# Performance work log

Measured on AMD Instinct MI355X. Metric: run time of the kernel, lower is better.

Reference implementation:

```python
import jax, jax.numpy as jnp
import numpy as np

THRESHOLD = 1.0
CURRENT_DECAY = 0.3
VOLTAGE_DECAY = 0.25
TAU_GRAD = 0.001  # surrogate-gradient sharpness (SLAYER escape-rate style)


@jax.custom_vjp
def spike(v):
    return (v >= THRESHOLD).astype(v.dtype)


def _spike_fwd(v):
    return spike(v), v


def _spike_bwd(v, g):
    # SLAYER-style surrogate: dS/dv = exp(-|v - theta| / tau) / tau
    return (g * jnp.exp(-jnp.abs(v - THRESHOLD) / TAU_GRAD) / TAU_GRAD,)


spike.defvjp(_spike_fwd, _spike_bwd)


def weight_norm(v, g):
    # torch weight_norm(dim=0): w = g * v / ||v|| with norm over all non-output dims
    axes = tuple(range(1, v.ndim))
    n = jnp.sqrt(jnp.sum(v * v, axis=axes, keepdims=True))
    return g.reshape((-1,) + (1,) * (v.ndim - 1)) * v / n


def cuba(z):
    # CUBA LIF dynamics over trailing time axis.  z: (B, ..., T)
    zt = jnp.moveaxis(z, -1, 0)  # (T, B, ...)

    def step(carry, z_t):
        c, v = carry
        c = (1.0 - CURRENT_DECAY) * c + z_t
        v = (1.0 - VOLTAGE_DECAY) * v + c
        s = spike(v)
        v = v * (1.0 - s)  # hard reset to zero on spike
        return (c, v), s

    init = (jnp.zeros_like(zt[0]), jnp.zeros_like(zt[0]))
    _, s = jax.lax.scan(step, init, zt)
    return jnp.moveaxis(s, 0, -1)  # (B, ..., T)


def conv2d_t(x, w):
    # Apply 2D conv independently per timestep. x: (B,C,H,W,T), w: (O,I,5,5)
    B, C, H, W, T = x.shape
    xb = jnp.moveaxis(x, -1, 1).reshape(B * T, C, H, W)
    y = jax.lax.conv_general_dilated(
        xb, w, window_strides=(4, 4), padding=[(1, 1), (1, 1)],
        dimension_numbers=('NCHW', 'OIHW', 'NCHW'))
    O, Ho, Wo = y.shape[1], y.shape[2], y.shape[3]
    return jnp.moveaxis(y.reshape(B, T, O, Ho, Wo), 1, -1)  # (B,O,Ho,Wo,T)


def dense_t(x, w):
    # x: (B, I, T), w: (O, I)
    return jnp.einsum('bit,oi->bot', x, w)


def setup_inputs() -> dict:
    key = jax.random.key(0)
    ks = jax.random.split(key, 8)
    B, T = 16, 64
    # sparse binary event input (DVS-like spikes)
    x = (jax.random.uniform(ks[0], (B, 2, 128, 128, T)) < 0.2).astype(jnp.float32)

    def mk(k, shape):
        fan_in = int(np.prod(shape[1:]))
        return jax.random.normal(k, shape, jnp.float32) / np.sqrt(fan_in)

    # weight_norm direction v; gain g absorbs weight_scale=2 (||w_eff|| = 2 per filter)
    return {
        'x': x,
        'conv1_v': mk(ks[1], (8, 2, 5, 5)),   'conv1_g': jnp.full((8,), 2.0, jnp.float32),
        'conv2_v': mk(ks[2], (32, 8, 5, 5)),  'conv2_g': jnp.full((32,), 2.0, jnp.float32),
        'conv3_v': mk(ks[3], (64, 32, 5, 5)), 'conv3_g': jnp.full((64,), 2.0, jnp.float32),
        'dense1_v': mk(ks[4], (2056, 256)),   'dense1_g': jnp.full((2056,), 2.0, jnp.float32),
        'dense2_v': mk(ks[5], (11, 2056)),    'dense2_g': jnp.full((11,), 2.0, jnp.float32),
    }


def reference(x, conv1_v, conv1_g, conv2_v, conv2_g, conv3_v, conv3_g,
              dense1_v, dense1_g, dense2_v, dense2_g):
    B = x.shape[0]
    T = x.shape[-1]
    # conv blocks: synapse then CUBA neuron
    for v, g in ((conv1_v, conv1_g), (conv2_v, conv2_g), (conv3_v, conv3_g)):
        x = cuba(conv2d_t(x, weight_norm(v, g)))
    # flatten (C,H,W) -> features; (B,64,2,2,T) -> (B,256,T)
    x = x.reshape(B, 64 * 2 * 2, T)
    for v, g in ((dense1_v, dense1_g), (dense2_v, dense2_g)):
        x = cuba(dense_t(x, weight_norm(v, g)))
    return x  # (B, 11, T) output spike train
```

## Files before the change

kernel.cpp:

```cpp
#include <hip/hip_runtime.h>
#include <cstddef>

#define TT 64

#define RFL(x) __builtin_amdgcn_readfirstlane(x)

typedef unsigned long long u64;

__device__ __forceinline__ void scanc(float& c, float& v, float& z) {
    c = fmaf(0.7f, c, z);
    v = fmaf(0.75f, v, c);
    float s = (v >= 1.0f) ? 1.0f : 0.0f;
    v = (v >= 1.0f) ? 0.0f : v;
    z = s;
}
__device__ __forceinline__ void scan4(float& c, float& v, float4& a) {
    scanc(c, v, a.x); scanc(c, v, a.y); scanc(c, v, a.z); scanc(c, v, a.w);
}
__device__ __forceinline__ float bit2f(u64 m, int t) {
    return (float)((m >> t) & 1ULL);
}

__global__ __launch_bounds__(256) void prep(
    const float* __restrict__ c1v, const float* __restrict__ c1g, float* __restrict__ w1T,
    const float* __restrict__ c2v, const float* __restrict__ c2g, float* __restrict__ w2T,
    const float* __restrict__ c3v, const float* __restrict__ c3g, float* __restrict__ w3T,
    const float* __restrict__ d1v, const float* __restrict__ d1g, float* __restrict__ wd1,
    const float* __restrict__ d2v, const float* __restrict__ d2g, float* __restrict__ wd2P,
    const float* __restrict__ x, u64* __restrict__ xb) {
    __shared__ float red[256];
    const int bid = blockIdx.x;
    if (bid >= 2171) {
        const int sub = threadIdx.x & 15;
        const int grp = threadIdx.x >> 4;
        const int pb = bid - 2171;
#pragma unroll
        for (int it = 0; it < 4; it++) {
            const size_t base = ((size_t)pb * 4 + it) * 32;
            const size_t p0 = base + grp;
            const size_t p1 = base + 16 + grp;
            const float4 v0 = *(const float4*)(x + p0 * TT + sub * 4);
            const float4 v1 = *(const float4*)(x + p1 * TT + sub * 4);
            const unsigned int n0 = (v0.x > 0.5f ? 1u : 0u) | (v0.y > 0.5f ? 2u : 0u) |
                                    (v0.z > 0.5f ? 4u : 0u) | (v0.w > 0.5f ? 8u : 0u);
            const unsigned int n1 = (v1.x > 0.5f ? 1u : 0u) | (v1.y > 0.5f ? 2u : 0u) |
                                    (v1.z > 0.5f ? 4u : 0u) | (v1.w > 0.5f ? 8u : 0u);
            u64 w0 = (u64)n0 << (4 * sub);
            u64 w1 = (u64)n1 << (4 * sub);
            w0 |= __shfl_xor(w0, 1); w1 |= __shfl_xor(w1, 1);
            w0 |= __shfl_xor(w0, 2); w1 |= __shfl_xor(w1, 2);
            w0 |= __shfl_xor(w0, 4); w1 |= __shfl_xor(w1, 4);
            w0 |= __shfl_xor(w0, 8); w1 |= __shfl_xor(w1, 8);
            if (sub == 0) { xb[p0] = w0; xb[p1] = w1; }
        }
        return;
    }
    const float *v, *g; float* w; int o, K, LD; bool tr;
    if (bid < 8)         { v = c1v; g = c1g; w = w1T;  o = bid;        K = 50;   LD = 8;  tr = true;  }
    else if (bid < 40)   { v = c2v; g = c2g; w = w2T;  o = bid - 8;    K = 200;  LD = 32; tr = true;  }
    else if (bid < 104)  { v = c3v; g = c3g; w = w3T;  o = bid - 40;   K = 800;  LD = 64; tr = true;  }
    else if (bid < 2160) { v = d1v; g = d1g; w = wd1;  o = bid - 104;  K = 256;  LD = 0;  tr = false; }
    else                 { v = d2v; g = d2g; w = wd2P; o = bid - 2160; K = 2056; LD = 12; tr = true;  }

    float s = 0.f;
    for (int k = threadIdx.x; k < K; k += 256) {
        float xx = v[(size_t)o * K + k];
        s += xx * xx;
    }
    red[threadIdx.x] = s;
    __syncthreads();
    for (int off = 128; off > 0; off >>= 1) {
        if (threadIdx.x < off) red[threadIdx.x] += red[threadIdx.x + off];
        __syncthreads();
    }
    const float scale = g[o] / sqrtf(red[0]);
    for (int k = threadIdx.x; k < K; k += 256) {
        float val = scale * v[(size_t)o * K + k];
        if (tr) w[(size_t)k * LD + o] = val;
        else    w[(size_t)o * K + k] = val;
    }
}

__global__ __launch_bounds__(256) void conv1_cuba(const u64* __restrict__ xb,
                                                  const float* __restrict__ w1T,
                                                  u64* __restrict__ s1b) {
    __shared__ float lds[4][8][68];
    const int wid = RFL(threadIdx.x >> 6), t = threadIdx.x & 63;
    const int task = RFL(blockIdx.x) * 4 + wid;
    const int spi = task & 1023, b = task >> 10;
    const int oy = spi >> 5, ox = spi & 31;

    float a0=0,a1=0,a2=0,a3=0,a4=0,a5=0,a6=0,a7=0;
    const u64* xq = xb + (size_t)b * 2 * 16384;

    if (oy >= 1 && ox >= 1) {
        const u64* xi = xq + (size_t)(oy * 4 - 1) * 128 + (ox * 4 - 1);
        for (int ci = 0; ci < 2; ci++) {
            u64 m[25];
#pragma unroll
            for (int ky = 0; ky < 5; ky++)
#pragma unroll
                for (int kx = 0; kx < 5; kx++)
                    m[ky * 5 + kx] = xi[ci * 16384 + ky * 128 + kx];
#pragma unroll
            for (int k = 0; k < 25; k++) {
                const float xvk = bit2f(m[k], t);
                const float4* wp = (const float4*)(w1T + (ci * 25 + k) * 8);
                const float4 wA = wp[0], wB = wp[1];
                a0 = fmaf(wA.x, xvk, a0); a1 = fmaf(wA.y, xvk, a1);
                a2 = fmaf(wA.z, xvk, a2); a3 = fmaf(wA.w, xvk, a3);
                a4 = fmaf(wB.x, xvk, a4); a5 = fmaf(wB.y, xvk, a5);
                a6 = fmaf(wB.z, xvk, a6); a7 = fmaf(wB.w, xvk, a7);
            }
        }
    } else {
        for (int ci = 0; ci < 2; ci++) {
#pragma unroll
            for (int ky = 0; ky < 5; ky++) {
                const int iy = oy * 4 + ky - 1;
                if (iy < 0 || iy >= 128) continue;
#pragma unroll
                for (int kx = 0; kx < 5; kx++) {
                    const int ix = ox * 4 + kx - 1;
                    if (ix < 0 || ix >= 128) continue;
                    const float xvk = bit2f(xq[ci * 16384 + iy * 128 + ix], t);
                    const float4* wp = (const float4*)(w1T + (ci * 25 + ky * 5 + kx) * 8);
                    const float4 wA = wp[0], wB = wp[1];
                    a0 = fmaf(wA.x, xvk, a0); a1 = fmaf(wA.y, xvk, a1);
                    a2 = fmaf(wA.z, xvk, a2); a3 = fmaf(wA.w, xvk, a3);
                    a4 = fmaf(wB.x, xvk, a4); a5 = fmaf(wB.y, xvk, a5);
                    a6 = fmaf(wB.z, xvk, a6); a7 = fmaf(wB.w, xvk, a7);
                }
            }
        }
    }
    lds[wid][0][t] = a0; lds[wid][1][t] = a1; lds[wid][2][t] = a2; lds[wid][3][t] = a3;
    lds[wid][4][t] = a4; lds[wid][5][t] = a5; lds[wid][6][t] = a6; lds[wid][7][t] = a7;
    __syncthreads();
    if (t < 8) {
        float* row = &lds[wid][t][0];
        float c = 0.f, v = 0.f;
        for (int tc = 0; tc < 4; tc++) {
            float4 r0 = *(const float4*)&row[tc * 16 + 0];
            float4 r1 = *(const float4*)&row[tc * 16 + 4];
            float4 r2 = *(const float4*)&row[tc * 16 + 8];
            float4 r3 = *(const float4*)&row[tc * 16 + 12];
            scan4(c, v, r0); scan4(c, v, r1); scan4(c, v, r2); scan4(c, v, r3);
            *(float4*)&row[tc * 16 + 0] = r0; *(float4*)&row[tc * 16 + 4] = r1;
            *(float4*)&row[tc * 16 + 8] = r2; *(float4*)&row[tc * 16 + 12] = r3;
        }
    }
    __syncthreads();
    u64* ob = s1b + (size_t)b * 8 * 1024 + spi;
#pragma unroll
    for (int ch = 0; ch < 8; ch++) {
        const u64 m = __ballot(lds[wid][ch][t] > 0.5f);
        if (t == 0) ob[(size_t)ch * 1024] = m;
    }
}

__global__ __launch_bounds__(256) void conv2_cuba(const u64* __restrict__ s1b,
                                                  const float* __restrict__ w2T,
                                                  float* __restrict__ s2) {
    __shared__ float lds[4][16][68];
    const int wid = RFL(threadIdx.x >> 6), t = threadIdx.x & 63;
    const int task = RFL(blockIdx.x) * 4 + wid;
    const int og = task & 1;
    const int spi = (task >> 1) & 63;
    const int b = task >> 7;
    const int oy = spi >> 3, ox = spi & 7;

    float a[16];
#pragma unroll
    for (int j = 0; j < 16; j++) a[j] = 0.f;
    const u64* sb = s1b + (size_t)b * 8 * 1024;

    if (oy >= 1 && ox >= 1) {
        const u64* si = sb + (size_t)(oy * 4 - 1) * 32 + (ox * 4 - 1);
        for (int ci = 0; ci < 8; ci++) {
            u64 m[25];
#pragma unroll
            for (int ky = 0; ky < 5; ky++)
#pragma unroll
                for (int kx = 0; kx < 5; kx++)
                    m[ky * 5 + kx] = si[ci * 1024 + ky * 32 + kx];
#pragma unroll
            for (int k = 0; k < 25; k++) {
                const float xvk = bit2f(m[k], t);
                const float4* wp = (const float4*)(w2T + (ci * 25 + k) * 32 + og * 16);
                const float4 w0 = wp[0], w1 = wp[1], w2 = wp[2], w3 = wp[3];
                a[0]  = fmaf(w0.x, xvk, a[0]);  a[1]  = fmaf(w0.y, xvk, a[1]);
                a[2]  = fmaf(w0.z, xvk, a[2]);  a[3]  = fmaf(w0.w, xvk, a[3]);
                a[4]  = fmaf(w1.x, xvk, a[4]);  a[5]  = fmaf(w1.y, xvk, a[5]);
                a[6]  = fmaf(w1.z, xvk, a[6]);  a[7]  = fmaf(w1.w, xvk, a[7]);
                a[8]  = fmaf(w2.x, xvk, a[8]);  a[9]  = fmaf(w2.y, xvk, a[9]);
                a[10] = fmaf(w2.z, xvk, a[10]); a[11] = fmaf(w2.w, xvk, a[11]);
                a[12] = fmaf(w3.x, xvk, a[12]); a[13] = fmaf(w3.y, xvk, a[13]);
                a[14] = fmaf(w3.z, xvk, a[14]); a[15] = fmaf(w3.w, xvk, a[15]);
            }
        }
    } else {
        for (int ci = 0; ci < 8; ci++) {
#pragma unroll
            for (int ky = 0; ky < 5; ky++) {
                const int iy = oy * 4 + ky - 1;
                if (iy < 0 || iy >= 32) continue;
#pragma unroll
                for (int kx = 0; kx < 5; kx++) {
                    const int ix = ox * 4 + kx - 1;
                    if (ix < 0 || ix >= 32) continue;
                    const float xvk = bit2f(sb[ci * 1024 + iy * 32 + ix], t);
                    const float4* wp =
                        (const float4*)(w2T + (ci * 25 + ky * 5 + kx) * 32 + og * 16);
                    const float4 w0 = wp[0], w1 = wp[1], w2 = wp[2], w3 = wp[3];
                    a[0]  = fmaf(w0.x, xvk, a[0]);  a[1]  = fmaf(w0.y, xvk, a[1]);
                    a[2]  = fmaf(w0.z, xvk, a[2]);  a[3]  = fmaf(w0.w, xvk, a[3]);
                    a[4]  = fmaf(w1.x, xvk, a[4]);  a[5]  = fmaf(w1.y, xvk, a[5]);
                    a[6]  = fmaf(w1.z, xvk, a[6]);  a[7]  = fmaf(w1.w, xvk, a[7]);
                    a[8]  = fmaf(w2.x, xvk, a[8]);  a[9]  = fmaf(w2.y, xvk, a[9]);
                    a[10] = fmaf(w2.z, xvk, a[10]); a[11] = fmaf(w2.w, xvk, a[11]);
                    a[12] = fmaf(w3.x, xvk, a[12]); a[13] = fmaf(w3.y, xvk, a[13]);
                    a[14] = fmaf(w3.z, xvk, a[14]); a[15] = fmaf(w3.w, xvk, a[15]);
                }
            }
        }
    }
#pragma unroll
    for (int j = 0; j < 16; j++) lds[wid][j][t] = a[j];
    __syncthreads();
    if (t < 16) {
        const float* row = &lds[wid][t][0];
        float4* op = (float4*)(s2 + (((size_t)b * 32 + og * 16 + t) * 64 + spi) * TT);
        float c = 0.f, v = 0.f;
        for (int tc = 0; tc < 4; tc++) {
            float4 r0 = *(const float4*)&row[tc * 16 + 0];
            float4 r1 = *(const float4*)&row[tc * 16 + 4];
            float4 r2 = *(const float4*)&row[tc * 16 + 8];
            float4 r3 = *(const float4*)&row[tc * 16 + 12];
            scan4(c, v, r0); scan4(c, v, r1); scan4(c, v, r2); scan4(c, v, r3);
            op[tc * 4 + 0] = r0; op[tc * 4 + 1] = r1;
            op[tc * 4 + 2] = r2; op[tc * 4 + 3] = r3;
        }
    }
}

template <int OY, int OX>
__device__ __forceinline__ void conv3_acc(const float* __restrict__ xb,
                                          const float* __restrict__ wTo,
                                          int wid, float* __restrict__ acc) {
    constexpr int KY0 = (OY == 0) ? 1 : 0;
    constexpr int KX0 = (OX == 0) ? 1 : 0;
    constexpr int NKY = 5 - KY0;
    constexpr int NKX = 5 - KX0;
    for (int c8 = 0; c8 < 8; c8++) {
        const int ci = wid * 8 + c8;
        float xv[NKY * NKX];
#pragma unroll
        for (int ky = KY0; ky < 5; ky++) {
#pragma unroll
            for (int kx = KX0; kx < 5; kx++) {
                const int iy = OY * 4 + ky - 1;
                const int ix = OX * 4 + kx - 1;
                xv[(ky - KY0) * NKX + (kx - KX0)] =
                    xb[((size_t)((ci * 8 + iy) * 8 + ix)) * TT];
            }
        }
#pragma unroll
        for (int ky = KY0; ky < 5; ky++) {
#pragma unroll
            for (int kx = KX0; kx < 5; kx++) {
                const float xvk = xv[(ky - KY0) * NKX + (kx - KX0)];
                const float4* wp = (const float4*)(wTo + (ci * 25 + ky * 5 + kx) * 64);
                const float4 wA = wp[0], wB = wp[1];
                acc[0] = fmaf(wA.x, xvk, acc[0]); acc[1] = fmaf(wA.y, xvk, acc[1]);
                acc[2] = fmaf(wA.z, xvk, acc[2]); acc[3] = fmaf(wA.w, xvk, acc[3]);
                acc[4] = fmaf(wB.x, xvk, acc[4]); acc[5] = fmaf(wB.y, xvk, acc[5]);
                acc[6] = fmaf(wB.z, xvk, acc[6]); acc[7] = fmaf(wB.w, xvk, acc[7]);
            }
        }
    }
}

__global__ __launch_bounds__(256) void conv3_cuba(const float* __restrict__ s2,
                                                  const float* __restrict__ wT,
                                                  float* __restrict__ s3) {
    __shared__ float red[4][8][68];
    const int wid = RFL(threadIdx.x >> 6), t = threadIdx.x & 63;
    const int og = RFL(blockIdx.x) & 7;
    const int spi = (RFL(blockIdx.x) >> 3) & 3;
    const int b = RFL(blockIdx.x) >> 5;

    float acc[8];
#pragma unroll
    for (int j = 0; j < 8; j++) acc[j] = 0.f;
    const float* xb = s2 + (size_t)b * 32 * 8 * 8 * TT + t;
    const float* wTo = wT + og * 8;

    switch (spi) {
        case 0: conv3_acc<0, 0>(xb, wTo, wid, acc); break;
        case 1: conv3_acc<0, 1>(xb, wTo, wid, acc); break;
        case 2: conv3_acc<1, 0>(xb, wTo, wid, acc); break;
        default: conv3_acc<1, 1>(xb, wTo, wid, acc); break;
    }
#pragma unroll
    for (int j = 0; j < 8; j++) red[wid][j][t] = acc[j];
    __syncthreads();
    if (wid == 0) {
#pragma unroll
        for (int j = 0; j < 8; j++)
            red[0][j][t] = ((red[0][j][t] + red[1][j][t]) + red[2][j][t]) + red[3][j][t];
    }
    __syncthreads();
    if (threadIdx.x < 8) {
        const int j = threadIdx.x;
        const float* row = &red[0][j][0];
        float4* op = (float4*)(s3 + ((size_t)b * 256 + og * 32 + j * 4 + spi) * TT);
        float c = 0.f, v = 0.f;
        for (int tc = 0; tc < 4; tc++) {
            float4 r0 = *(const float4*)&row[tc * 16 + 0];
            float4 r1 = *(const float4*)&row[tc * 16 + 4];
            float4 r2 = *(const float4*)&row[tc * 16 + 8];
            float4 r3 = *(const float4*)&row[tc * 16 + 12];
            scan4(c, v, r0); scan4(c, v, r1); scan4(c, v, r2); scan4(c, v, r3);
            op[tc * 4 + 0] = r0; op[tc * 4 + 1] = r1;
            op[tc * 4 + 2] = r2; op[tc * 4 + 3] = r3;
        }
    }
}

__global__ __launch_bounds__(256) void dense1_cuba(const float* __restrict__ s3,
                                                   const float* __restrict__ w,
                                                   float* __restrict__ s4) {
    __shared__ float lds[4][8][68];
    const int wid = threadIdx.x >> 6, t = threadIdx.x & 63;
    const int task = blockIdx.x * 4 + wid;
    const int bq = task / 257;
    const int ogq = task - bq * 257;
    const int b = RFL(bq);
    const int o0 = RFL(ogq * 8);

    float a0=0,a1=0,a2=0,a3=0,a4=0,a5=0,a6=0,a7=0;
    const float* ab = s3 + (size_t)b * 256 * TT + t;
    const float* r0 = w + (size_t)(o0 + 0) * 256;
    const float* r1 = w + (size_t)(o0 + 1) * 256;
    const float* r2 = w + (size_t)(o0 + 2) * 256;
    const float* r3 = w + (size_t)(o0 + 3) * 256;
    const float* r4 = w + (size_t)(o0 + 4) * 256;
    const float* r5 = w + (size_t)(o0 + 5) * 256;
    const float* r6 = w + (size_t)(o0 + 6) * 256;
    const float* r7 = w + (size_t)(o0 + 7) * 256;

#pragma unroll 2
    for (int i = 0; i < 256; i += 4) {
        const float av0 = ab[(size_t)(i + 0) * TT];
        const float av1 = ab[(size_t)(i + 1) * TT];
        const float av2 = ab[(size_t)(i + 2) * TT];
        const float av3 = ab[(size_t)(i + 3) * TT];
        const float4 q0 = *(const float4*)(r0 + i);
        const float4 q1 = *(const float4*)(r1 + i);
        const float4 q2 = *(const float4*)(r2 + i);
        const float4 q3 = *(const float4*)(r3 + i);
        const float4 q4 = *(const float4*)(r4 + i);
        const float4 q5 = *(const float4*)(r5 + i);
        const float4 q6 = *(const float4*)(r6 + i);
        const float4 q7 = *(const float4*)(r7 + i);
        a0 = fmaf(q0.x, av0, a0); a1 = fmaf(q1.x, av0, a1);
        a2 = fmaf(q2.x, av0, a2); a3 = fmaf(q3.x, av0, a3);
        a4 = fmaf(q4.x, av0, a4); a5 = fmaf(q5.x, av0, a5);
        a6 = fmaf(q6.x, av0, a6); a7 = fmaf(q7.x, av0, a7);
        a0 = fmaf(q0.y, av1, a0); a1 = fmaf(q1.y, av1, a1);
        a2 = fmaf(q2.y, av1, a2); a3 = fmaf(q3.y, av1, a3);
        a4 = fmaf(q4.y, av1, a4); a5 = fmaf(q5.y, av1, a5);
        a6 = fmaf(q6.y, av1, a6); a7 = fmaf(q7.y, av1, a7);
        a0 = fmaf(q0.z, av2, a0); a1 = fmaf(q1.z, av2, a1);
        a2 = fmaf(q2.z, av2, a2); a3 = fmaf(q3.z, av2, a3);
        a4 = fmaf(q4.z, av2, a4); a5 = fmaf(q5.z, av2, a5);
        a6 = fmaf(q6.z, av2, a6); a7 = fmaf(q7.z, av2, a7);
        a0 = fmaf(q0.w, av3, a0); a1 = fmaf(q1.w, av3, a1);
        a2 = fmaf(q2.w, av3, a2); a3 = fmaf(q3.w, av3, a3);
        a4 = fmaf(q4.w, av3, a4); a5 = fmaf(q5.w, av3, a5);
        a6 = fmaf(q6.w, av3, a6); a7 = fmaf(q7.w, av3, a7);
    }
    lds[wid][0][t] = a0; lds[wid][1][t] = a1; lds[wid][2][t] = a2; lds[wid][3][t] = a3;
    lds[wid][4][t] = a4; lds[wid][5][t] = a5; lds[wid][6][t] = a6; lds[wid][7][t] = a7;
    __syncthreads();
    if (t < 8) {
        const float* row = &lds[wid][t][0];
        float4* op = (float4*)(s4 + ((size_t)b * 2056 + o0 + t) * TT);
        float c = 0.f, v = 0.f;
        for (int tc = 0; tc < 4; tc++) {
            float4 r0q = *(const float4*)&row[tc * 16 + 0];
            float4 r1q = *(const float4*)&row[tc * 16 + 4];
            float4 r2q = *(const float4*)&row[tc * 16 + 8];
            float4 r3q = *(const float4*)&row[tc * 16 + 12];
            scan4(c, v, r0q); scan4(c, v, r1q); scan4(c, v, r2q); scan4(c, v, r3q);
            op[tc * 4 + 0] = r0q; op[tc * 4 + 1] = r1q;
            op[tc * 4 + 2] = r2q; op[tc * 4 + 3] = r3q;
        }
    }
}

__global__ __launch_bounds__(256) void dense2_part(const float* __restrict__ s4,
                                                   const float* __restrict__ wP,
                                                   float* __restrict__ z4p) {
    __shared__ float red[4][11][64];
    const int sp = blockIdx.x, b = blockIdx.y;
    const int w = threadIdx.x >> 6, t = threadIdx.x & 63;
    const int i0 = sp * 129;
    const int iend = (i0 + 129 < 2056) ? i0 + 129 : 2056;
    const float* src = s4 + (size_t)b * 2056 * TT + t;

    float acc[11];
#pragma unroll
    for (int j = 0; j < 11; j++) acc[j] = 0.f;

#pragma unroll 4
    for (int i = i0 + w; i < iend; i += 4) {
        const float xv = src[(size_t)i * TT];
        const float4* wp = (const float4*)(wP + (size_t)i * 12);
        const float4 w0 = wp[0], w1 = wp[1], w2 = wp[2];
        acc[0]  = fmaf(w0.x, xv, acc[0]);  acc[1]  = fmaf(w0.y, xv, acc[1]);
        acc[2]  = fmaf(w0.z, xv, acc[2]);  acc[3]  = fmaf(w0.w, xv, acc[3]);
        acc[4]  = fmaf(w1.x, xv, acc[4]);  acc[5]  = fmaf(w1.y, xv, acc[5]);
        acc[6]  = fmaf(w1.z, xv, acc[6]);  acc[7]  = fmaf(w1.w, xv, acc[7]);
        acc[8]  = fmaf(w2.x, xv, acc[8]);  acc[9]  = fmaf(w2.y, xv, acc[9]);
        acc[10] = fmaf(w2.z, xv, acc[10]);
    }
#pragma unroll
    for (int j = 0; j < 11; j++) red[w][j][t] = acc[j];
    __syncthreads();
    if (w == 0) {
#pragma unroll
        for (int j = 0; j < 11; j++) {
            const float s = red[0][j][t] + red[1][j][t] + red[2][j][t] + red[3][j][t];
            z4p[(((size_t)b * 16 + sp) * 11 + j) * TT + t] = s;
        }
    }
}

__global__ __launch_bounds__(256) void dense2_scan(const float* __restrict__ z4p,
                                                   float* __restrict__ out) {
    __shared__ float z[11][64];
    const int b = blockIdx.x;
    for (int idx = threadIdx.x; idx < 11 * 64; idx += 256) {
        const int o = idx >> 6, t = idx & 63;
        float s = 0.f;
#pragma unroll
        for (int sp = 0; sp < 16; sp++)
            s += z4p[(((size_t)b * 16 + sp) * 11 + o) * TT + t];
        z[o][t] = s;
    }
    __syncthreads();
    if (threadIdx.x < 11) {
        const int o = threadIdx.x;
        float c = 0.f, v = 0.f;
        float* op = out + ((size_t)b * 11 + o) * TT;
#pragma unroll
        for (int t = 0; t < TT; t++) {
            float zz = z[o][t];
            scanc(c, v, zz);
            op[t] = zz;
        }
    }
}

extern "C" void kernel_launch(void* const* d_in, const int* in_sizes, int n_in,
                              void* d_out, int out_size, void* d_ws, size_t ws_size,
                              hipStream_t stream) {
    const float* x   = (const float*)d_in[0];
    const float* c1v = (const float*)d_in[1];  const float* c1g = (const float*)d_in[2];
    const float* c2v = (const float*)d_in[3];  const float* c2g = (const float*)d_in[4];
    const float* c3v = (const float*)d_in[5];  const float* c3g = (const float*)d_in[6];
    const float* d1v = (const float*)d_in[7];  const float* d1g = (const float*)d_in[8];
    const float* d2v = (const float*)d_in[9];  const float* d2g = (const float*)d_in[10];

    float* ws = (float*)d_ws;
    float* w1T  = ws + 0;
    float* w2T  = ws + 400;
    float* w3T  = ws + 6800;
    float* wd1  = ws + 58000;
    float* wd2P = ws + 584336;
    float* A = ws + 609008;
    float* B = A + 8388608;
    float* s3  = A;
    float* s4  = A + 262144;
    float* s2  = B;
    float* z4p = B + 2097152;
    u64* xbits  = (u64*)(ws + 13191920);
    u64* s1bits = (u64*)(ws + 14240496);
    (void)ws_size; (void)in_sizes; (void)n_in; (void)out_size;

    prep<<<dim3(2171 + 4096), dim3(256), 0, stream>>>(
        c1v, c1g, w1T, c2v, c2g, w2T, c3v, c3g, w3T, d1v, d1g, wd1,
        d2v, d2g, wd2P, x, xbits);

    conv1_cuba <<<dim3(4096),   dim3(256), 0, stream>>>(xbits, w1T, s1bits);
    conv2_cuba <<<dim3(512),    dim3(256), 0, stream>>>(s1bits, w2T, s2);
    conv3_cuba <<<dim3(512),    dim3(256), 0, stream>>>(s2, w3T, s3);
    dense1_cuba<<<dim3(1028),   dim3(256), 0, stream>>>(s3, wd1, s4);
    dense2_part<<<dim3(16, 16), dim3(256), 0, stream>>>(s4, wd2P, z4p);
    dense2_scan<<<dim3(16),     dim3(256), 0, stream>>>(z4p, (float*)d_out);
}
```

Baseline: 152.9 us.

## Pack intermediate spike trains as 64-bit masks across conv2..dense2

Conv2, conv3 and dense1 now write their spike outputs as one 64-bit ballot mask per neuron (one bit per timestep) instead of 64 floats, and the consuming kernels extract the bit per lane. This cuts intermediate global traffic for s2, s3 and s4 by a factor of 32 and shrinks the workspace. In exchange it adds an extra LDS round trip plus a barrier and ballot loop in each producer, and a shift and convert per input in the consumers.

```diff
diff --git a/kernel.cpp b/kernel.cpp
--- a/kernel.cpp
+++ b/kernel.cpp
@@ -161,7 +161,7 @@
 
 __global__ __launch_bounds__(256) void conv2_cuba(const u64* __restrict__ s1b,
                                                   const float* __restrict__ w2T,
-                                                  float* __restrict__ s2) {
+                                                  u64* __restrict__ s2b) {
     __shared__ float lds[4][16][68];
     const int wid = RFL(threadIdx.x >> 6), t = threadIdx.x & 63;
     const int task = RFL(blockIdx.x) * 4 + wid;
@@ -229,8 +229,7 @@
     for (int j = 0; j < 16; j++) lds[wid][j][t] = a[j];
     __syncthreads();
     if (t < 16) {
-        const float* row = &lds[wid][t][0];
-        float4* op = (float4*)(s2 + (((size_t)b * 32 + og * 16 + t) * 64 + spi) * TT);
+        float* row = &lds[wid][t][0];
         float c = 0.f, v = 0.f;
         for (int tc = 0; tc < 4; tc++) {
             float4 r0 = *(const float4*)&row[tc * 16 + 0];
@@ -238,14 +237,21 @@
             float4 r2 = *(const float4*)&row[tc * 16 + 8];
             float4 r3 = *(const float4*)&row[tc * 16 + 12];
             scan4(c, v, r0); scan4(c, v, r1); scan4(c, v, r2); scan4(c, v, r3);
-            op[tc * 4 + 0] = r0; op[tc * 4 + 1] = r1;
-            op[tc * 4 + 2] = r2; op[tc * 4 + 3] = r3;
-        }
+            *(float4*)&row[tc * 16 + 0] = r0; *(float4*)&row[tc * 16 + 4] = r1;
+            *(float4*)&row[tc * 16 + 8] = r2; *(float4*)&row[tc * 16 + 12] = r3;
+        }
+    }
+    __syncthreads();
+    u64* ob = s2b + (size_t)b * 2048 + (size_t)(og * 16) * 64 + spi;
+#pragma unroll
+    for (int ch = 0; ch < 16; ch++) {
+        const u64 m = __ballot(lds[wid][ch][t] > 0.5f);
+        if (t == 0) ob[(size_t)ch * 64] = m;
     }
 }
 
 template <int OY, int OX>
-__device__ __forceinline__ void conv3_acc(const float* __restrict__ xb,
+__device__ __forceinline__ void conv3_acc(const u64* __restrict__ xq, int t,
                                           const float* __restrict__ wTo,
                                           int wid, float* __restrict__ acc) {
     constexpr int KY0 = (OY == 0) ? 1 : 0;
@@ -254,22 +260,21 @@
     constexpr int NKX = 5 - KX0;
     for (int c8 = 0; c8 < 8; c8++) {
         const int ci = wid * 8 + c8;
-        float xv[NKY * NKX];
+        u64 m[NKY * NKX];
 #pragma unroll
         for (int ky = KY0; ky < 5; ky++) {
 #pragma unroll
             for (int kx = KX0; kx < 5; kx++) {
                 const int iy = OY * 4 + ky - 1;
                 const int ix = OX * 4 + kx - 1;
-                xv[(ky - KY0) * NKX + (kx - KX0)] =
-                    xb[((size_t)((ci * 8 + iy) * 8 + ix)) * TT];
+                m[(ky - KY0) * NKX + (kx - KX0)] = xq[ci * 64 + iy * 8 + ix];
             }
         }
 #pragma unroll
         for (int ky = KY0; ky < 5; ky++) {
 #pragma unroll
             for (int kx = KX0; kx < 5; kx++) {
-                const float xvk = xv[(ky - KY0) * NKX + (kx - KX0)];
+                const float xvk = bit2f(m[(ky - KY0) * NKX + (kx - KX0)], t);
                 const float4* wp = (const float4*)(wTo + (ci * 25 + ky * 5 + kx) * 64);
                 const float4 wA = wp[0], wB = wp[1];
                 acc[0] = fmaf(wA.x, xvk, acc[0]); acc[1] = fmaf(wA.y, xvk, acc[1]);
@@ -281,9 +286,9 @@
     }
 }
 
-__global__ __launch_bounds__(256) void conv3_cuba(const float* __restrict__ s2,
+__global__ __launch_bounds__(256) void conv3_cuba(const u64* __restrict__ s2b,
                                                   const float* __restrict__ wT,
-                                                  float* __restrict__ s3) {
+                                                  u64* __restrict__ s3b) {
     __shared__ float red[4][8][68];
     const int wid = RFL(threadIdx.x >> 6), t = threadIdx.x & 63;
     const int og = RFL(blockIdx.x) & 7;
@@ -293,14 +298,14 @@
     float acc[8];
 #pragma unroll
     for (int j = 0; j < 8; j++) acc[j] = 0.f;
-    const float* xb = s2 + (size_t)b * 32 * 8 * 8 * TT + t;
+    const u64* xq = s2b + (size_t)b * 2048;
     const float* wTo = wT + og * 8;
 
     switch (spi) {
-        case 0: conv3_acc<0, 0>(xb, wTo, wid, acc); break;
-        case 1: conv3_acc<0, 1>(xb, wTo, wid, acc); break;
-        case 2: conv3_acc<1, 0>(xb, wTo, wid, acc); break;
-        default: conv3_acc<1, 1>(xb, wTo, wid, acc); break;
+        case 0: conv3_acc<0, 0>(xq, t, wTo, wid, acc); break;
+        case 1: conv3_acc<0, 1>(xq, t, wTo, wid, acc); break;
+        case 2: conv3_acc<1, 0>(xq, t, wTo, wid, acc); break;
+        default: conv3_acc<1, 1>(xq, t, wTo, wid, acc); break;
     }
 #pragma unroll
     for (int j = 0; j < 8; j++) red[wid][j][t] = acc[j];
@@ -311,26 +316,32 @@
             red[0][j][t] = ((red[0][j][t] + red[1][j][t]) + red[2][j][t]) + red[3][j][t];
     }
     __syncthreads();
-    if (threadIdx.x < 8) {
-        const int j = threadIdx.x;
-        const float* row = &red[0][j][0];
-        float4* op = (float4*)(s3 + ((size_t)b * 256 + og * 32 + j * 4 + spi) * TT);
-        float c = 0.f, v = 0.f;
-        for (int tc = 0; tc < 4; tc++) {
-            float4 r0 = *(const float4*)&row[tc * 16 + 0];
-            float4 r1 = *(const float4*)&row[tc * 16 + 4];
-            float4 r2 = *(const float4*)&row[tc * 16 + 8];
-            float4 r3 = *(const float4*)&row[tc * 16 + 12];
-            scan4(c, v, r0); scan4(c, v, r1); scan4(c, v, r2); scan4(c, v, r3);
-            op[tc * 4 + 0] = r0; op[tc * 4 + 1] = r1;
-            op[tc * 4 + 2] = r2; op[tc * 4 + 3] = r3;
-        }
-    }
-}
-
-__global__ __launch_bounds__(256) void dense1_cuba(const float* __restrict__ s3,
+    if (wid == 0) {
+        if (t < 8) {
+            float* row = &red[0][t][0];
+            float c = 0.f, v = 0.f;
+            for (int tc = 0; tc < 4; tc++) {
+                float4 r0 = *(const float4*)&row[tc * 16 + 0];
+                float4 r1 = *(const float4*)&row[tc * 16 + 4];
+                float4 r2 = *(const float4*)&row[tc * 16 + 8];
+                float4 r3 = *(const float4*)&row[tc * 16 + 12];
+                scan4(c, v, r0); scan4(c, v, r1); scan4(c, v, r2); scan4(c, v, r3);
+                *(float4*)&row[tc * 16 + 0] = r0; *(float4*)&row[tc * 16 + 4] = r1;
+                *(float4*)&row[tc * 16 + 8] = r2; *(float4*)&row[tc * 16 + 12] = r3;
+            }
+        }
+        u64* ob = s3b + (size_t)b * 256 + og * 32 + spi;
+#pragma unroll
+        for (int j = 0; j < 8; j++) {
+            const u64 m = __ballot(red[0][j][t] > 0.5f);
+            if (t == 0) ob[(size_t)j * 4] = m;
+        }
+    }
+}
+
+__global__ __launch_bounds__(256) void dense1_cuba(const u64* __restrict__ s3b,
                                                    const float* __restrict__ w,
-                                                   float* __restrict__ s4) {
+                                                   u64* __restrict__ s4b) {
     __shared__ float lds[4][8][68];
     const int wid = threadIdx.x >> 6, t = threadIdx.x & 63;
     const int task = blockIdx.x * 4 + wid;
@@ -340,7 +351,7 @@
     const int o0 = RFL(ogq * 8);
 
     float a0=0,a1=0,a2=0,a3=0,a4=0,a5=0,a6=0,a7=0;
-    const float* ab = s3 + (size_t)b * 256 * TT + t;
+    const u64* ab = s3b + (size_t)b * 256;
     const float* r0 = w + (size_t)(o0 + 0) * 256;
     const float* r1 = w + (size_t)(o0 + 1) * 256;
     const float* r2 = w + (size_t)(o0 + 2) * 256;
@@ -352,10 +363,11 @@
 
 #pragma unroll 2
     for (int i = 0; i < 256; i += 4) {
-        const float av0 = ab[(size_t)(i + 0) * TT];
-        const float av1 = ab[(size_t)(i + 1) * TT];
-        const float av2 = ab[(size_t)(i + 2) * TT];
-        const float av3 = ab[(size_t)(i + 3) * TT];
+        const u64 m0 = ab[i + 0], m1 = ab[i + 1], m2 = ab[i + 2], m3 = ab[i + 3];
+        const float av0 = bit2f(m0, t);
+        const float av1 = bit2f(m1, t);
+        const float av2 = bit2f(m2, t);
+        const float av3 = bit2f(m3, t);
         const float4 q0 = *(const float4*)(r0 + i);
         const float4 q1 = *(const float4*)(r1 + i);
         const float4 q2 = *(const float4*)(r2 + i);
@@ -385,8 +397,7 @@
     lds[wid][4][t] = a4; lds[wid][5][t] = a5; lds[wid][6][t] = a6; lds[wid][7][t] = a7;
     __syncthreads();
     if (t < 8) {
-        const float* row = &lds[wid][t][0];
-        float4* op = (float4*)(s4 + ((size_t)b * 2056 + o0 + t) * TT);
+        float* row = &lds[wid][t][0];
         float c = 0.f, v = 0.f;
         for (int tc = 0; tc < 4; tc++) {
             float4 r0q = *(const float4*)&row[tc * 16 + 0];
@@ -394,13 +405,19 @@
             float4 r2q = *(const float4*)&row[tc * 16 + 8];
             float4 r3q = *(const float4*)&row[tc * 16 + 12];
             scan4(c, v, r0q); scan4(c, v, r1q); scan4(c, v, r2q); scan4(c, v, r3q);
-            op[tc * 4 + 0] = r0q; op[tc * 4 + 1] = r1q;
-            op[tc * 4 + 2] = r2q; op[tc * 4 + 3] = r3q;
-        }
-    }
-}
-
-__global__ __launch_bounds__(256) void dense2_part(const float* __restrict__ s4,
+            *(float4*)&row[tc * 16 + 0] = r0q; *(float4*)&row[tc * 16 + 4] = r1q;
+            *(float4*)&row[tc * 16 + 8] = r2q; *(float4*)&row[tc * 16 + 12] = r3q;
+        }
+    }
+    u64* ob = s4b + (size_t)b * 2056 + o0;
+#pragma unroll
+    for (int ch = 0; ch < 8; ch++) {
+        const u64 m = __ballot(lds[wid][ch][t] > 0.5f);
+        if (t == 0) ob[ch] = m;
+    }
+}
+
+__global__ __launch_bounds__(256) void dense2_part(const u64* __restrict__ s4b,
                                                    const float* __restrict__ wP,
                                                    float* __restrict__ z4p) {
     __shared__ float red[4][11][64];
@@ -408,7 +425,7 @@
     const int w = threadIdx.x >> 6, t = threadIdx.x & 63;
     const int i0 = sp * 129;
     const int iend = (i0 + 129 < 2056) ? i0 + 129 : 2056;
-    const float* src = s4 + (size_t)b * 2056 * TT + t;
+    const u64* src = s4b + (size_t)b * 2056;
 
     float acc[11];
 #pragma unroll
@@ -416,7 +433,7 @@
 
 #pragma unroll 4
     for (int i = i0 + w; i < iend; i += 4) {
-        const float xv = src[(size_t)i * TT];
+        const float xv = bit2f(src[i], t);
         const float4* wp = (const float4*)(wP + (size_t)i * 12);
         const float4 w0 = wp[0], w1 = wp[1], w2 = wp[2];
         acc[0]  = fmaf(w0.x, xv, acc[0]);  acc[1]  = fmaf(w0.y, xv, acc[1]);
@@ -480,14 +497,12 @@
     float* w3T  = ws + 6800;
     float* wd1  = ws + 58000;
     float* wd2P = ws + 584336;
-    float* A = ws + 609008;
-    float* B = A + 8388608;
-    float* s3  = A;
-    float* s4  = A + 262144;
-    float* s2  = B;
-    float* z4p = B + 2097152;
-    u64* xbits  = (u64*)(ws + 13191920);
-    u64* s1bits = (u64*)(ws + 14240496);
+    float* z4p  = ws + 609008;
+    u64* xbits  = (u64*)(ws + 789232);
+    u64* s1bits = (u64*)(ws + 1837808);
+    u64* s2bits = (u64*)(ws + 2099952);
+    u64* s3bits = (u64*)(ws + 2165488);
+    u64* s4bits = (u64*)(ws + 2173680);
     (void)ws_size; (void)in_sizes; (void)n_in; (void)out_size;
 
     prep<<<dim3(2171 + 4096), dim3(256), 0, stream>>>(
@@ -495,9 +510,9 @@
         d2v, d2g, wd2P, x, xbits);
 
     conv1_cuba <<<dim3(4096),   dim3(256), 0, stream>>>(xbits, w1T, s1bits);
-    conv2_cuba <<<dim3(512),    dim3(256), 0, stream>>>(s1bits, w2T, s2);
-    conv3_cuba <<<dim3(512),    dim3(256), 0, stream>>>(s2, w3T, s3);
-    dense1_cuba<<<dim3(1028),   dim3(256), 0, stream>>>(s3, wd1, s4);
-    dense2_part<<<dim3(16, 16), dim3(256), 0, stream>>>(s4, wd2P, z4p);
+    conv2_cuba <<<dim3(512),    dim3(256), 0, stream>>>(s1bits, w2T, s2bits);
+    conv3_cuba <<<dim3(512),    dim3(256), 0, stream>>>(s2bits, w3T, s3bits);
+    dense1_cuba<<<dim3(1028),   dim3(256), 0, stream>>>(s3bits, wd1, s4bits);
+    dense2_part<<<dim3(16, 16), dim3(256), 0, stream>>>(s4bits, wd2P, z4p);
     dense2_scan<<<dim3(16),     dim3(256), 0, stream>>>(z4p, (float*)d_out);
 }
```

After: 160.1 us. 4.7% more time.
